# Performance work log

Hardware: AMD Instinct MI355X
Metric: run time of the kernel (lower is better)

Reference implementation:

```python
import jax, jax.numpy as jnp
import numpy as np

B, T, F = 1024, 512, 64
H1, H2, D1, D2, NOUT = 32, 16, 16, 8, 1


def setup_inputs() -> dict:
    key = jax.random.key(0)
    ks = jax.random.split(key, 14)
    s = lambda k, shape, fan: jax.random.normal(k, shape, jnp.float32) / np.sqrt(fan)
    return {
        "x": jax.random.normal(ks[0], (B, T, F), jnp.float32),
        "Wx1": s(ks[1], (F, H1), F),
        "Wh1": s(ks[2], (H1, H1), H1),
        "b1": jnp.zeros((H1,), jnp.float32),
        "Wx2": s(ks[3], (H1, H2), H1),
        "Wh2": s(ks[4], (H2, H2), H2),
        "b2": jnp.zeros((H2,), jnp.float32),
        "W3": s(ks[5], (H2, D1), H2),
        "b3": jnp.zeros((D1,), jnp.float32),
        "W4": s(ks[6], (D1, D2), D1),
        "b4": jnp.zeros((D2,), jnp.float32),
        "Wo": s(ks[7], (D2, NOUT), D2),
        "bo": jnp.zeros((NOUT,), jnp.float32),
    }


def reference(x, Wx1, Wh1, b1, Wx2, Wh2, b2, W3, b3, W4, b4, Wo, bo):
    b = x.shape[0]
    # SimpleRNN 1 (return_sequences=True): h_t = tanh(x_t Wx + h_{t-1} Wh + b)
    # Precompute input projection for all timesteps: [T, B, H1]
    xp1 = jnp.swapaxes(jnp.einsum('btf,fh->bth', x, Wx1) + b1, 0, 1)

    def step1(h, xt):
        h = jnp.tanh(xt + h @ Wh1)
        return h, h

    _, seq1 = jax.lax.scan(step1, jnp.zeros((b, Wh1.shape[0]), x.dtype), xp1)
    # SimpleRNN 2 (return_sequences=False): keep only final state
    xp2 = seq1 @ Wx2 + b2  # [T, B, H2]

    def step2(h, xt):
        h = jnp.tanh(xt + h @ Wh2)
        return h, None

    h2, _ = jax.lax.scan(step2, jnp.zeros((b, Wh2.shape[0]), x.dtype), xp2)
    # Dense head
    y = jax.nn.relu(h2 @ W3 + b3)
    y = y @ W4 + b4
    return y @ Wo + bo
```

## Files before the change

### kernel.cpp

```cpp
#include <hip/hip_runtime.h>

#define BB 1024
#define TB 512
#define FB 64
#define NH1 32
#define NH2 16
#define ND1 16
#define ND2 8

#define RD 16
#define RDM (RD - 1)
#define CHUNK 8
#define NCH (TB / CHUNK)

#define WAVE_FENCE() __builtin_amdgcn_fence(__ATOMIC_ACQ_REL, "wavefront")

__device__ __forceinline__ float tanh_fast(float v) {
    float e = __expf(2.0f * v);
    return fmaf(-2.0f, __builtin_amdgcn_rcpf(e + 1.0f), 1.0f);
}

__global__ __attribute__((amdgpu_flat_work_group_size(192, 192)))
           __attribute__((amdgpu_waves_per_eu(3)))
void rnn_pipe_kernel(
    const float* __restrict__ x,
    const float* __restrict__ Wx1, const float* __restrict__ Wh1, const float* __restrict__ b1,
    const float* __restrict__ Wx2, const float* __restrict__ Wh2, const float* __restrict__ b2,
    const float* __restrict__ W3,  const float* __restrict__ b3,
    const float* __restrict__ W4,  const float* __restrict__ b4,
    const float* __restrict__ Wo,  const float* __restrict__ bo,
    float* __restrict__ out)
{
    __shared__ __align__(16) float xs[CHUNK][FB];
    __shared__ __align__(16) float xpring[RD][NH1];
    __shared__ __align__(16) float h1ring[RD][NH1];
    __shared__ __align__(16) float h2s[NH2];
    __shared__ __align__(16) float ys[ND1];

    const int tid  = threadIdx.x;
    const int wid  = tid >> 6;
    const int lane = tid & 63;
    const int h = lane & 31;
    const int p = lane >> 5;
    const int g = lane & 15;
    const int q = lane >> 4;
    const int b = blockIdx.x;

    if (wid == 0) {
        auto w1 = [&](int i) { return Wx1[(32 * p + i) * NH1 + h]; };
        const float4 wxa = make_float4(w1(0),  w1(1),  w1(2),  w1(3));
        const float4 wxb = make_float4(w1(4),  w1(5),  w1(6),  w1(7));
        const float4 wxc = make_float4(w1(8),  w1(9),  w1(10), w1(11));
        const float4 wxd = make_float4(w1(12), w1(13), w1(14), w1(15));
        const float4 wxe = make_float4(w1(16), w1(17), w1(18), w1(19));
        const float4 wxf = make_float4(w1(20), w1(21), w1(22), w1(23));
        const float4 wxg = make_float4(w1(24), w1(25), w1(26), w1(27));
        const float4 wxh = make_float4(w1(28), w1(29), w1(30), w1(31));
        const float b1v = (p == 0) ? b1[h] : 0.0f;

        const float* xb = x + (size_t)b * TB * FB + lane;
        float xq0 = xb[0 * FB];
        float xq1 = xb[1 * FB];
        float xq2 = xb[2 * FB];
        float xq3 = xb[3 * FB];
        float xq4 = xb[4 * FB];
        float xq5 = xb[5 * FB];
        float xq6 = xb[6 * FB];
        float xq7 = xb[7 * FB];

#define XPSTEP(S, T0)                                                          \
    {                                                                          \
        const int t_ = (T0) + (S);                                             \
        const float4* xv = (const float4*)&xs[S][32 * p];                      \
        float a0 = b1v, a1 = 0.0f, a2 = 0.0f, a3 = 0.0f;                       \
        float4 v_;                                                             \
        v_ = xv[0]; a0 = fmaf(v_.x, wxa.x, a0); a1 = fmaf(v_.y, wxa.y, a1);    \
                    a2 = fmaf(v_.z, wxa.z, a2); a3 = fmaf(v_.w, wxa.w, a3);    \
        v_ = xv[1]; a0 = fmaf(v_.x, wxb.x, a0); a1 = fmaf(v_.y, wxb.y, a1);    \
                    a2 = fmaf(v_.z, wxb.z, a2); a3 = fmaf(v_.w, wxb.w, a3);    \
        v_ = xv[2]; a0 = fmaf(v_.x, wxc.x, a0); a1 = fmaf(v_.y, wxc.y, a1);    \
                    a2 = fmaf(v_.z, wxc.z, a2); a3 = fmaf(v_.w, wxc.w, a3);    \
        v_ = xv[3]; a0 = fmaf(v_.x, wxd.x, a0); a1 = fmaf(v_.y, wxd.y, a1);    \
                    a2 = fmaf(v_.z, wxd.z, a2); a3 = fmaf(v_.w, wxd.w, a3);    \
        v_ = xv[4]; a0 = fmaf(v_.x, wxe.x, a0); a1 = fmaf(v_.y, wxe.y, a1);    \
                    a2 = fmaf(v_.z, wxe.z, a2); a3 = fmaf(v_.w, wxe.w, a3);    \
        v_ = xv[5]; a0 = fmaf(v_.x, wxf.x, a0); a1 = fmaf(v_.y, wxf.y, a1);    \
                    a2 = fmaf(v_.z, wxf.z, a2); a3 = fmaf(v_.w, wxf.w, a3);    \
        v_ = xv[6]; a0 = fmaf(v_.x, wxg.x, a0); a1 = fmaf(v_.y, wxg.y, a1);    \
                    a2 = fmaf(v_.z, wxg.z, a2); a3 = fmaf(v_.w, wxg.w, a3);    \
        v_ = xv[7]; a0 = fmaf(v_.x, wxh.x, a0); a1 = fmaf(v_.y, wxh.y, a1);    \
                    a2 = fmaf(v_.z, wxh.z, a2); a3 = fmaf(v_.w, wxh.w, a3);    \
        float acc = (a0 + a1) + (a2 + a3);                                     \
        acc += __shfl_xor(acc, 32, 64);                                        \
        WAVE_FENCE();                                                          \
        if (p == 0) xpring[t_ & RDM][h] = acc;                                 \
    }

        for (int c = 0; c < NCH + 2; ++c) {
            if (c < NCH) {
                const int t0 = c * CHUNK;
                xs[0][lane] = xq0;
                xs[1][lane] = xq1;
                xs[2][lane] = xq2;
                xs[3][lane] = xq3;
                xs[4][lane] = xq4;
                xs[5][lane] = xq5;
                xs[6][lane] = xq6;
                xs[7][lane] = xq7;
                {
                    const int nb = (c + 1) * CHUNK;
                    int n0 = nb + 0; n0 = (n0 < TB) ? n0 : (TB - 1);
                    int n1 = nb + 1; n1 = (n1 < TB) ? n1 : (TB - 1);
                    int n2 = nb + 2; n2 = (n2 < TB) ? n2 : (TB - 1);
                    int n3 = nb + 3; n3 = (n3 < TB) ? n3 : (TB - 1);
                    int n4 = nb + 4; n4 = (n4 < TB) ? n4 : (TB - 1);
                    int n5 = nb + 5; n5 = (n5 < TB) ? n5 : (TB - 1);
                    int n6 = nb + 6; n6 = (n6 < TB) ? n6 : (TB - 1);
                    int n7 = nb + 7; n7 = (n7 < TB) ? n7 : (TB - 1);
                    xq0 = xb[(size_t)n0 * FB];
                    xq1 = xb[(size_t)n1 * FB];
                    xq2 = xb[(size_t)n2 * FB];
                    xq3 = xb[(size_t)n3 * FB];
                    xq4 = xb[(size_t)n4 * FB];
                    xq5 = xb[(size_t)n5 * FB];
                    xq6 = xb[(size_t)n6 * FB];
                    xq7 = xb[(size_t)n7 * FB];
                }
                XPSTEP(0, t0); XPSTEP(1, t0); XPSTEP(2, t0); XPSTEP(3, t0);
                XPSTEP(4, t0); XPSTEP(5, t0); XPSTEP(6, t0); XPSTEP(7, t0);
            }
            __syncthreads();
        }
#undef XPSTEP

    } else if (wid == 1) {
        auto r1f = [&](int j) { return Wh1[j * NH1 + h]; };
        const float4 whA = make_float4(r1f(0),  r1f(1),  r1f(2),  r1f(3));
        const float4 whB = make_float4(r1f(4),  r1f(5),  r1f(6),  r1f(7));
        const float4 whC = make_float4(r1f(8),  r1f(9),  r1f(10), r1f(11));
        const float4 whD = make_float4(r1f(12), r1f(13), r1f(14), r1f(15));
        const float4 whE = make_float4(r1f(16), r1f(17), r1f(18), r1f(19));
        const float4 whF = make_float4(r1f(20), r1f(21), r1f(22), r1f(23));
        const float4 whG = make_float4(r1f(24), r1f(25), r1f(26), r1f(27));
        const float4 whH = make_float4(r1f(28), r1f(29), r1f(30), r1f(31));

        if (p == 0) h1ring[RDM][h] = 0.0f;

#define L1S(S, T0)                                                             \
    {                                                                          \
        const int t_ = (T0) + (S);                                             \
        float xpv = xpring[t_ & RDM][h];                                       \
        const float4* hr = (const float4*)&h1ring[(t_ - 1) & RDM][0];          \
        float4 r0 = hr[0], r1 = hr[1], r2 = hr[2], r3 = hr[3];                 \
        float4 r4 = hr[4], r5 = hr[5], r6 = hr[6], r7 = hr[7];                 \
        float a0 = xpv,  a1 = 0.0f, a2 = 0.0f, a3 = 0.0f;                      \
        float a4 = 0.0f, a5 = 0.0f, a6 = 0.0f, a7 = 0.0f;                      \
        a0 = fmaf(r0.x, whA.x, a0); a1 = fmaf(r0.y, whA.y, a1);                \
        a2 = fmaf(r0.z, whA.z, a2); a3 = fmaf(r0.w, whA.w, a3);                \
        a4 = fmaf(r1.x, whB.x, a4); a5 = fmaf(r1.y, whB.y, a5);                \
        a6 = fmaf(r1.z, whB.z, a6); a7 = fmaf(r1.w, whB.w, a7);                \
        a0 = fmaf(r2.x, whC.x, a0); a1 = fmaf(r2.y, whC.y, a1);                \
        a2 = fmaf(r2.z, whC.z, a2); a3 = fmaf(r2.w, whC.w, a3);                \
        a4 = fmaf(r3.x, whD.x, a4); a5 = fmaf(r3.y, whD.y, a5);                \
        a6 = fmaf(r3.z, whD.z, a6); a7 = fmaf(r3.w, whD.w, a7);                \
        a0 = fmaf(r4.x, whE.x, a0); a1 = fmaf(r4.y, whE.y, a1);                \
        a2 = fmaf(r4.z, whE.z, a2); a3 = fmaf(r4.w, whE.w, a3);                \
        a4 = fmaf(r5.x, whF.x, a4); a5 = fmaf(r5.y, whF.y, a5);                \
        a6 = fmaf(r5.z, whF.z, a6); a7 = fmaf(r5.w, whF.w, a7);                \
        a0 = fmaf(r6.x, whG.x, a0); a1 = fmaf(r6.y, whG.y, a1);                \
        a2 = fmaf(r6.z, whG.z, a2); a3 = fmaf(r6.w, whG.w, a3);                \
        a4 = fmaf(r7.x, whH.x, a4); a5 = fmaf(r7.y, whH.y, a5);                \
        a6 = fmaf(r7.z, whH.z, a6); a7 = fmaf(r7.w, whH.w, a7);                \
        float acc = ((a0 + a1) + (a2 + a3)) + ((a4 + a5) + (a6 + a7));         \
        float h1new = tanh_fast(acc);                                          \
        WAVE_FENCE();                                                          \
        if (p == 0) h1ring[t_ & RDM][h] = h1new;                               \
        WAVE_FENCE();                                                          \
    }

        for (int c = 0; c < NCH + 2; ++c) {
            if (c >= 1 && c <= NCH) {
                const int t0 = (c - 1) * CHUNK;
                L1S(0, t0); L1S(1, t0); L1S(2, t0); L1S(3, t0);
                L1S(4, t0); L1S(5, t0); L1S(6, t0); L1S(7, t0);
            }
            __syncthreads();
        }
#undef L1S

    } else {
        auto w2f = [&](int i) { return Wx2[(8 * q + i) * NH2 + g]; };
        const float4 o2a = make_float4(w2f(0), w2f(1), w2f(2), w2f(3));
        const float4 o2b = make_float4(w2f(4), w2f(5), w2f(6), w2f(7));
        auto r2f = [&](int j) { return Wh2[j * NH2 + g]; };
        const float4 w2A = make_float4(r2f(0),  r2f(1),  r2f(2),  r2f(3));
        const float4 w2B = make_float4(r2f(4),  r2f(5),  r2f(6),  r2f(7));
        const float4 w2C = make_float4(r2f(8),  r2f(9),  r2f(10), r2f(11));
        const float4 w2D = make_float4(r2f(12), r2f(13), r2f(14), r2f(15));
        const float b2v = (q == 0) ? b2[g] : 0.0f;

        if (lane < NH2) h2s[lane] = 0.0f;

#define L2S(S, T0)                                                             \
    {                                                                          \
        const int t_ = (T0) + (S);                                             \
        const float* hrow = &h1ring[t_ & RDM][8 * q];                          \
        float4 u0 = *(const float4*)(hrow);                                    \
        float4 u1 = *(const float4*)(hrow + 4);                                \
        const float4* hv = (const float4*)h2s;                                 \
        float4 v0 = hv[0], v1 = hv[1], v2 = hv[2], v3 = hv[3];                 \
        float cu0 = b2v, cu1 = 0.0f;                                           \
        cu0 = fmaf(u0.x, o2a.x, cu0); cu1 = fmaf(u0.y, o2a.y, cu1);            \
        cu0 = fmaf(u0.z, o2a.z, cu0); cu1 = fmaf(u0.w, o2a.w, cu1);            \
        cu0 = fmaf(u1.x, o2b.x, cu0); cu1 = fmaf(u1.y, o2b.y, cu1);            \
        cu0 = fmaf(u1.z, o2b.z, cu0); cu1 = fmaf(u1.w, o2b.w, cu1);            \
        float cu = cu0 + cu1;                                                  \
        cu += __shfl_xor(cu, 16, 64);                                          \
        cu += __shfl_xor(cu, 32, 64);                                          \
        float c0 = 0.0f, c1 = 0.0f, c2 = 0.0f, c3 = 0.0f;                      \
        c0 = fmaf(v0.x, w2A.x, c0); c1 = fmaf(v0.y, w2A.y, c1);                \
        c2 = fmaf(v0.z, w2A.z, c2); c3 = fmaf(v0.w, w2A.w, c3);                \
        c0 = fmaf(v1.x, w2B.x, c0); c1 = fmaf(v1.y, w2B.y, c1);                \
        c2 = fmaf(v1.z, w2B.z, c2); c3 = fmaf(v1.w, w2B.w, c3);                \
        c0 = fmaf(v2.x, w2C.x, c0); c1 = fmaf(v2.y, w2C.y, c1);                \
        c2 = fmaf(v2.z, w2C.z, c2); c3 = fmaf(v2.w, w2C.w, c3);                \
        c0 = fmaf(v3.x, w2D.x, c0); c1 = fmaf(v3.y, w2D.y, c1);                \
        c2 = fmaf(v3.z, w2D.z, c2); c3 = fmaf(v3.w, w2D.w, c3);                \
        float ch = (c0 + c1) + (c2 + c3);                                      \
        float h2new = tanh_fast(cu + ch);                                      \
        WAVE_FENCE();                                                          \
        if (lane < NH2) h2s[lane] = h2new;                                     \
        WAVE_FENCE();                                                          \
    }

        for (int c = 0; c < NCH + 2; ++c) {
            if (c >= 2) {
                const int t0 = (c - 2) * CHUNK;
                L2S(0, t0); L2S(1, t0); L2S(2, t0); L2S(3, t0);
                L2S(4, t0); L2S(5, t0); L2S(6, t0); L2S(7, t0);
            }
            __syncthreads();
        }
#undef L2S

        WAVE_FENCE();
        float a3h = b3[g];
#pragma unroll
        for (int j = 0; j < 16; ++j) a3h = fmaf(h2s[j], W3[j * ND1 + g], a3h);
        float y1 = fmaxf(a3h, 0.0f);
        WAVE_FENCE();
        if (lane < ND1) ys[lane] = y1;
        WAVE_FENCE();

        const int e = lane & 7;
        float a4 = b4[e];
#pragma unroll
        for (int j = 0; j < 16; ++j) a4 = fmaf(ys[j], W4[j * ND2 + e], a4);

        float yo = a4 * Wo[e];
        yo += __shfl_xor(yo, 1, 64);
        yo += __shfl_xor(yo, 2, 64);
        yo += __shfl_xor(yo, 4, 64);
        if (lane == 0) out[b] = yo + bo[0];
    }
}

extern "C" void kernel_launch(void* const* d_in, const int* in_sizes, int n_in,
                              void* d_out, int out_size, void* d_ws, size_t ws_size,
                              hipStream_t stream) {
    const float* x   = (const float*)d_in[0];
    const float* Wx1 = (const float*)d_in[1];
    const float* Wh1 = (const float*)d_in[2];
    const float* b1  = (const float*)d_in[3];
    const float* Wx2 = (const float*)d_in[4];
    const float* Wh2 = (const float*)d_in[5];
    const float* b2  = (const float*)d_in[6];
    const float* W3  = (const float*)d_in[7];
    const float* b3  = (const float*)d_in[8];
    const float* W4  = (const float*)d_in[9];
    const float* b4  = (const float*)d_in[10];
    const float* Wo  = (const float*)d_in[11];
    const float* bo  = (const float*)d_in[12];
    float* out = (float*)d_out;

    rnn_pipe_kernel<<<dim3(BB), dim3(192), 0, stream>>>(
        x, Wx1, Wh1, b1, Wx2, Wh2, b2, W3, b3, W4, b4, Wo, bo, out);
}
```

Before: 335.1 us.

## Keep recurrent hidden states in registers via readlane; load x directly from global

The recurrent hidden states of both RNN layers now live in registers. Each step broadcasts them with readlane instead of writing to and re-reading from shared memory, which removes per-step LDS round trips and wave fences from the serial critical path. The projection wave now reads x straight from global memory as float4 instead of staging it through shared memory with prefetch registers. It also writes both half-sums to the ring so the consumer adds them, dropping a cross-lane shuffle. The risks are exposed global load latency in the producer wave and scalar readlane serialization in the recurrence.

```diff
diff --git a/kernel.cpp b/kernel.cpp
--- a/kernel.cpp
+++ b/kernel.cpp
@@ -18,6 +18,10 @@
 __device__ __forceinline__ float tanh_fast(float v) {
     float e = __expf(2.0f * v);
     return fmaf(-2.0f, __builtin_amdgcn_rcpf(e + 1.0f), 1.0f);
+}
+
+__device__ __forceinline__ float rdl(float v, int l) {
+    return __int_as_float(__builtin_amdgcn_readlane(__float_as_int(v), l));
 }
 
 __global__ __attribute__((amdgpu_flat_work_group_size(192, 192)))
@@ -31,11 +35,8 @@
     const float* __restrict__ Wo,  const float* __restrict__ bo,
     float* __restrict__ out)
 {
-    __shared__ __align__(16) float xs[CHUNK][FB];
-    __shared__ __align__(16) float xpring[RD][NH1];
+    __shared__ __align__(16) float xpring[RD][2 * NH1];
     __shared__ __align__(16) float h1ring[RD][NH1];
-    __shared__ __align__(16) float h2s[NH2];
-    __shared__ __align__(16) float ys[ND1];
 
     const int tid  = threadIdx.x;
     const int wid  = tid >> 6;
@@ -58,20 +59,12 @@
         const float4 wxh = make_float4(w1(28), w1(29), w1(30), w1(31));
         const float b1v = (p == 0) ? b1[h] : 0.0f;
 
-        const float* xb = x + (size_t)b * TB * FB + lane;
-        float xq0 = xb[0 * FB];
-        float xq1 = xb[1 * FB];
-        float xq2 = xb[2 * FB];
-        float xq3 = xb[3 * FB];
-        float xq4 = xb[4 * FB];
-        float xq5 = xb[5 * FB];
-        float xq6 = xb[6 * FB];
-        float xq7 = xb[7 * FB];
+        const float* xbase = x + (size_t)b * TB * FB + 32 * p;
 
 #define XPSTEP(S, T0)                                                          \
     {                                                                          \
         const int t_ = (T0) + (S);                                             \
-        const float4* xv = (const float4*)&xs[S][32 * p];                      \
+        const float4* xv = (const float4*)(xbase + (size_t)t_ * FB);           \
         float a0 = b1v, a1 = 0.0f, a2 = 0.0f, a3 = 0.0f;                       \
         float4 v_;                                                             \
         v_ = xv[0]; a0 = fmaf(v_.x, wxa.x, a0); a1 = fmaf(v_.y, wxa.y, a1);    \
@@ -90,42 +83,13 @@
                     a2 = fmaf(v_.z, wxg.z, a2); a3 = fmaf(v_.w, wxg.w, a3);    \
         v_ = xv[7]; a0 = fmaf(v_.x, wxh.x, a0); a1 = fmaf(v_.y, wxh.y, a1);    \
                     a2 = fmaf(v_.z, wxh.z, a2); a3 = fmaf(v_.w, wxh.w, a3);    \
-        float acc = (a0 + a1) + (a2 + a3);                                     \
-        acc += __shfl_xor(acc, 32, 64);                                        \
-        WAVE_FENCE();                                                          \
-        if (p == 0) xpring[t_ & RDM][h] = acc;                                 \
+        float part = (a0 + a1) + (a2 + a3);                                    \
+        xpring[t_ & RDM][lane] = part;                                         \
     }
 
         for (int c = 0; c < NCH + 2; ++c) {
             if (c < NCH) {
                 const int t0 = c * CHUNK;
-                xs[0][lane] = xq0;
-                xs[1][lane] = xq1;
-                xs[2][lane] = xq2;
-                xs[3][lane] = xq3;
-                xs[4][lane] = xq4;
-                xs[5][lane] = xq5;
-                xs[6][lane] = xq6;
-                xs[7][lane] = xq7;
-                {
-                    const int nb = (c + 1) * CHUNK;
-                    int n0 = nb + 0; n0 = (n0 < TB) ? n0 : (TB - 1);
-                    int n1 = nb + 1; n1 = (n1 < TB) ? n1 : (TB - 1);
-                    int n2 = nb + 2; n2 = (n2 < TB) ? n2 : (TB - 1);
-                    int n3 = nb + 3; n3 = (n3 < TB) ? n3 : (TB - 1);
-                    int n4 = nb + 4; n4 = (n4 < TB) ? n4 : (TB - 1);
-                    int n5 = nb + 5; n5 = (n5 < TB) ? n5 : (TB - 1);
-                    int n6 = nb + 6; n6 = (n6 < TB) ? n6 : (TB - 1);
-                    int n7 = nb + 7; n7 = (n7 < TB) ? n7 : (TB - 1);
-                    xq0 = xb[(size_t)n0 * FB];
-                    xq1 = xb[(size_t)n1 * FB];
-                    xq2 = xb[(size_t)n2 * FB];
-                    xq3 = xb[(size_t)n3 * FB];
-                    xq4 = xb[(size_t)n4 * FB];
-                    xq5 = xb[(size_t)n5 * FB];
-                    xq6 = xb[(size_t)n6 * FB];
-                    xq7 = xb[(size_t)n7 * FB];
-                }
                 XPSTEP(0, t0); XPSTEP(1, t0); XPSTEP(2, t0); XPSTEP(3, t0);
                 XPSTEP(4, t0); XPSTEP(5, t0); XPSTEP(6, t0); XPSTEP(7, t0);
             }
@@ -143,73 +107,71 @@
         const float4 whF = make_float4(r1f(20), r1f(21), r1f(22), r1f(23));
         const float4 whG = make_float4(r1f(24), r1f(25), r1f(26), r1f(27));
         const float4 whH = make_float4(r1f(28), r1f(29), r1f(30), r1f(31));
-
-        if (p == 0) h1ring[RDM][h] = 0.0f;
-
-#define L1S(S, T0)                                                             \
+        float h1v = 0.0f;
+
+#define RL4(J, WV)                                                             \
+        { float s0_ = rdl(h1v, (J)+0); float s1_ = rdl(h1v, (J)+1);            \
+          float s2_ = rdl(h1v, (J)+2); float s3_ = rdl(h1v, (J)+3);            \
+          a0 = fmaf(s0_, WV.x, a0); a1 = fmaf(s1_, WV.y, a1);                  \
+          a2 = fmaf(s2_, WV.z, a2); a3 = fmaf(s3_, WV.w, a3); }
+
+#define L1S(XPV, T)                                                            \
     {                                                                          \
-        const int t_ = (T0) + (S);                                             \
-        float xpv = xpring[t_ & RDM][h];                                       \
-        const float4* hr = (const float4*)&h1ring[(t_ - 1) & RDM][0];          \
-        float4 r0 = hr[0], r1 = hr[1], r2 = hr[2], r3 = hr[3];                 \
-        float4 r4 = hr[4], r5 = hr[5], r6 = hr[6], r7 = hr[7];                 \
-        float a0 = xpv,  a1 = 0.0f, a2 = 0.0f, a3 = 0.0f;                      \
-        float a4 = 0.0f, a5 = 0.0f, a6 = 0.0f, a7 = 0.0f;                      \
-        a0 = fmaf(r0.x, whA.x, a0); a1 = fmaf(r0.y, whA.y, a1);                \
-        a2 = fmaf(r0.z, whA.z, a2); a3 = fmaf(r0.w, whA.w, a3);                \
-        a4 = fmaf(r1.x, whB.x, a4); a5 = fmaf(r1.y, whB.y, a5);                \
-        a6 = fmaf(r1.z, whB.z, a6); a7 = fmaf(r1.w, whB.w, a7);                \
-        a0 = fmaf(r2.x, whC.x, a0); a1 = fmaf(r2.y, whC.y, a1);                \
-        a2 = fmaf(r2.z, whC.z, a2); a3 = fmaf(r2.w, whC.w, a3);                \
-        a4 = fmaf(r3.x, whD.x, a4); a5 = fmaf(r3.y, whD.y, a5);                \
-        a6 = fmaf(r3.z, whD.z, a6); a7 = fmaf(r3.w, whD.w, a7);                \
-        a0 = fmaf(r4.x, whE.x, a0); a1 = fmaf(r4.y, whE.y, a1);                \
-        a2 = fmaf(r4.z, whE.z, a2); a3 = fmaf(r4.w, whE.w, a3);                \
-        a4 = fmaf(r5.x, whF.x, a4); a5 = fmaf(r5.y, whF.y, a5);                \
-        a6 = fmaf(r5.z, whF.z, a6); a7 = fmaf(r5.w, whF.w, a7);                \
-        a0 = fmaf(r6.x, whG.x, a0); a1 = fmaf(r6.y, whG.y, a1);                \
-        a2 = fmaf(r6.z, whG.z, a2); a3 = fmaf(r6.w, whG.w, a3);                \
-        a4 = fmaf(r7.x, whH.x, a4); a5 = fmaf(r7.y, whH.y, a5);                \
-        a6 = fmaf(r7.z, whH.z, a6); a7 = fmaf(r7.w, whH.w, a7);                \
-        float acc = ((a0 + a1) + (a2 + a3)) + ((a4 + a5) + (a6 + a7));         \
-        float h1new = tanh_fast(acc);                                          \
+        float a0 = (XPV), a1 = 0.0f, a2 = 0.0f, a3 = 0.0f;                     \
+        RL4(0,  whA) RL4(4,  whB) RL4(8,  whC) RL4(12, whD)                    \
+        RL4(16, whE) RL4(20, whF) RL4(24, whG) RL4(28, whH)                    \
+        float acc = (a0 + a1) + (a2 + a3);                                     \
+        h1v = tanh_fast(acc);                                                  \
         WAVE_FENCE();                                                          \
-        if (p == 0) h1ring[t_ & RDM][h] = h1new;                               \
+        if (p == 0) h1ring[(T) & RDM][h] = h1v;                                \
         WAVE_FENCE();                                                          \
     }
 
         for (int c = 0; c < NCH + 2; ++c) {
             if (c >= 1 && c <= NCH) {
                 const int t0 = (c - 1) * CHUNK;
-                L1S(0, t0); L1S(1, t0); L1S(2, t0); L1S(3, t0);
-                L1S(4, t0); L1S(5, t0); L1S(6, t0); L1S(7, t0);
+                float xp0 = xpring[(t0+0) & RDM][h] + xpring[(t0+0) & RDM][h+32];
+                float xp1 = xpring[(t0+1) & RDM][h] + xpring[(t0+1) & RDM][h+32];
+                float xp2 = xpring[(t0+2) & RDM][h] + xpring[(t0+2) & RDM][h+32];
+                float xp3 = xpring[(t0+3) & RDM][h] + xpring[(t0+3) & RDM][h+32];
+                float xp4 = xpring[(t0+4) & RDM][h] + xpring[(t0+4) & RDM][h+32];
+                float xp5 = xpring[(t0+5) & RDM][h] + xpring[(t0+5) & RDM][h+32];
+                float xp6 = xpring[(t0+6) & RDM][h] + xpring[(t0+6) & RDM][h+32];
+                float xp7 = xpring[(t0+7) & RDM][h] + xpring[(t0+7) & RDM][h+32];
+                L1S(xp0, t0 + 0); L1S(xp1, t0 + 1);
+                L1S(xp2, t0 + 2); L1S(xp3, t0 + 3);
+                L1S(xp4, t0 + 4); L1S(xp5, t0 + 5);
+                L1S(xp6, t0 + 6); L1S(xp7, t0 + 7);
             }
             __syncthreads();
         }
 #undef L1S
+#undef RL4
 
     } else {
         auto w2f = [&](int i) { return Wx2[(8 * q + i) * NH2 + g]; };
         const float4 o2a = make_float4(w2f(0), w2f(1), w2f(2), w2f(3));
         const float4 o2b = make_float4(w2f(4), w2f(5), w2f(6), w2f(7));
-        auto r2f = [&](int j) { return Wh2[j * NH2 + g]; };
+        auto r2f = [&](int k) { return Wh2[k * NH2 + g]; };
         const float4 w2A = make_float4(r2f(0),  r2f(1),  r2f(2),  r2f(3));
         const float4 w2B = make_float4(r2f(4),  r2f(5),  r2f(6),  r2f(7));
         const float4 w2C = make_float4(r2f(8),  r2f(9),  r2f(10), r2f(11));
         const float4 w2D = make_float4(r2f(12), r2f(13), r2f(14), r2f(15));
-        const float b2v = (q == 0) ? b2[g] : 0.0f;
-
-        if (lane < NH2) h2s[lane] = 0.0f;
-
-#define L2S(S, T0)                                                             \
+        const float b2v = b2[g];
+        float h2v = 0.0f;
+
+#define RL4H(J, WV)                                                            \
+        { float s0_ = rdl(h2v, (J)+0); float s1_ = rdl(h2v, (J)+1);            \
+          float s2_ = rdl(h2v, (J)+2); float s3_ = rdl(h2v, (J)+3);            \
+          c0 = fmaf(s0_, WV.x, c0); c1 = fmaf(s1_, WV.y, c1);                  \
+          c2 = fmaf(s2_, WV.z, c2); c3 = fmaf(s3_, WV.w, c3); }
+
+#define L2S(T)                                                                 \
     {                                                                          \
-        const int t_ = (T0) + (S);                                             \
-        const float* hrow = &h1ring[t_ & RDM][8 * q];                          \
+        const float* hrow = &h1ring[(T) & RDM][8 * q];                         \
         float4 u0 = *(const float4*)(hrow);                                    \
         float4 u1 = *(const float4*)(hrow + 4);                                \
-        const float4* hv = (const float4*)h2s;                                 \
-        float4 v0 = hv[0], v1 = hv[1], v2 = hv[2], v3 = hv[3];                 \
-        float cu0 = b2v, cu1 = 0.0f;                                           \
+        float cu0 = 0.0f, cu1 = 0.0f;                                          \
         cu0 = fmaf(u0.x, o2a.x, cu0); cu1 = fmaf(u0.y, o2a.y, cu1);            \
         cu0 = fmaf(u0.z, o2a.z, cu0); cu1 = fmaf(u0.w, o2a.w, cu1);            \
         cu0 = fmaf(u1.x, o2b.x, cu0); cu1 = fmaf(u1.y, o2b.y, cu1);            \
@@ -217,45 +179,32 @@
         float cu = cu0 + cu1;                                                  \
         cu += __shfl_xor(cu, 16, 64);                                          \
         cu += __shfl_xor(cu, 32, 64);                                          \
-        float c0 = 0.0f, c1 = 0.0f, c2 = 0.0f, c3 = 0.0f;                      \
-        c0 = fmaf(v0.x, w2A.x, c0); c1 = fmaf(v0.y, w2A.y, c1);                \
-        c2 = fmaf(v0.z, w2A.z, c2); c3 = fmaf(v0.w, w2A.w, c3);                \
-        c0 = fmaf(v1.x, w2B.x, c0); c1 = fmaf(v1.y, w2B.y, c1);                \
-        c2 = fmaf(v1.z, w2B.z, c2); c3 = fmaf(v1.w, w2B.w, c3);                \
-        c0 = fmaf(v2.x, w2C.x, c0); c1 = fmaf(v2.y, w2C.y, c1);                \
-        c2 = fmaf(v2.z, w2C.z, c2); c3 = fmaf(v2.w, w2C.w, c3);                \
-        c0 = fmaf(v3.x, w2D.x, c0); c1 = fmaf(v3.y, w2D.y, c1);                \
-        c2 = fmaf(v3.z, w2D.z, c2); c3 = fmaf(v3.w, w2D.w, c3);                \
+        float c0 = b2v, c1 = 0.0f, c2 = 0.0f, c3 = 0.0f;                       \
+        RL4H(0, w2A) RL4H(4, w2B) RL4H(8, w2C) RL4H(12, w2D)                   \
         float ch = (c0 + c1) + (c2 + c3);                                      \
-        float h2new = tanh_fast(cu + ch);                                      \
-        WAVE_FENCE();                                                          \
-        if (lane < NH2) h2s[lane] = h2new;                                     \
-        WAVE_FENCE();                                                          \
+        h2v = tanh_fast(cu + ch);                                              \
     }
 
         for (int c = 0; c < NCH + 2; ++c) {
             if (c >= 2) {
                 const int t0 = (c - 2) * CHUNK;
-                L2S(0, t0); L2S(1, t0); L2S(2, t0); L2S(3, t0);
-                L2S(4, t0); L2S(5, t0); L2S(6, t0); L2S(7, t0);
+                L2S(t0 + 0); L2S(t0 + 1); L2S(t0 + 2); L2S(t0 + 3);
+                L2S(t0 + 4); L2S(t0 + 5); L2S(t0 + 6); L2S(t0 + 7);
             }
             __syncthreads();
         }
 #undef L2S
-
-        WAVE_FENCE();
+#undef RL4H
+
         float a3h = b3[g];
 #pragma unroll
-        for (int j = 0; j < 16; ++j) a3h = fmaf(h2s[j], W3[j * ND1 + g], a3h);
+        for (int j = 0; j < 16; ++j) a3h = fmaf(rdl(h2v, j), W3[j * ND1 + g], a3h);
         float y1 = fmaxf(a3h, 0.0f);
-        WAVE_FENCE();
-        if (lane < ND1) ys[lane] = y1;
-        WAVE_FENCE();
 
         const int e = lane & 7;
         float a4 = b4[e];
 #pragma unroll
-        for (int j = 0; j < 16; ++j) a4 = fmaf(ys[j], W4[j * ND2 + e], a4);
+        for (int j = 0; j < 16; ++j) a4 = fmaf(rdl(y1, j), W4[j * ND2 + e], a4);
 
         float yo = a4 * Wo[e];
         yo += __shfl_xor(yo, 1, 64);
```

After: 535.7 us. 59.8% more time.
